# Kernel tuning notes

Hardware: AMD Instinct MI355X
Metric: run time of the kernel (lower is better)

The kernel has to match this reference:

```python
import jax, jax.numpy as jnp
import numpy as np
from jax import lax

T_ITERS = 6
LN_EPS = 1e-5

def layer_norm(x, g, b):
    mu = jnp.mean(x, axis=-1, keepdims=True)
    var = jnp.var(x, axis=-1, keepdims=True)
    return (x - mu) * lax.rsqrt(var + LN_EPS) * g + b

def setup_inputs() -> dict:
    key = jax.random.key(0)
    ks = jax.random.split(key, 12)
    B, C_in, S = 8, 128, 33
    hidden = 2 * C_in          # 256
    dim = 256                  # feat_dim
    N = 64
    w = lambda k, shp, s=0.02: (jax.random.normal(k, shp, jnp.float32) * s)
    return {
        "x": jax.random.normal(ks[0], (B, C_in, S, S, S), jnp.float32),
        "templates_init": jax.random.normal(ks[1], (1, N, dim), jnp.float32),
        "conv_w": w(ks[2], (hidden, C_in, 3, 3, 3)),
        "conv_b": jnp.zeros((hidden,), jnp.float32),
        "Wq": w(ks[3], (dim, dim)),
        "Wk": w(ks[4], (hidden, dim)),
        "Wv": w(ks[5], (hidden, dim)),
        "ln_in_g": jnp.ones((hidden,), jnp.float32), "ln_in_b": jnp.zeros((hidden,), jnp.float32),
        "ln_t_g": jnp.ones((dim,), jnp.float32),    "ln_t_b": jnp.zeros((dim,), jnp.float32),
        "ln_m_g": jnp.ones((dim,), jnp.float32),    "ln_m_b": jnp.zeros((dim,), jnp.float32),
        "W1": w(ks[6], (dim, 2 * dim)), "b1": jnp.zeros((2 * dim,), jnp.float32),
        "W2": w(ks[7], (2 * dim, dim)), "b2": jnp.zeros((dim,), jnp.float32),
    }

def reference(x, templates_init, conv_w, conv_b, Wq, Wk, Wv,
              ln_in_g, ln_in_b, ln_t_g, ln_t_b, ln_m_g, ln_m_b,
              W1, b1, W2, b2):
    # project: Conv3d stride 2, no padding, + ReLU
    h = lax.conv_general_dilated(x, conv_w, window_strides=(2, 2, 2),
                                 padding='VALID',
                                 dimension_numbers=('NCDHW', 'OIDHW', 'NCDHW'))
    h = jax.nn.relu(h + conv_b[None, :, None, None, None])
    B, C, X, Y, Z = h.shape
    dim = templates_init.shape[-1]
    N = templates_init.shape[1]
    scale = dim ** (-0.5)
    tokens = h.reshape(B, C, X * Y * Z).transpose(0, 2, 1)   # (B, L, hidden)
    tokens = layer_norm(tokens, ln_in_g, ln_in_b)
    k = tokens @ Wk                                           # (B, L, dim)
    v = tokens @ Wv                                           # (B, L, dim)
    templates = jnp.broadcast_to(templates_init, (B, N, dim))
    attn = None
    for _ in range(T_ITERS):
        t_prev = templates
        t = layer_norm(templates, ln_t_g, ln_t_b)
        q = (t @ Wq) * scale                                  # (B, N, dim)
        attn_logits = jnp.einsum('bnd,bld->bln', q, k)        # (B, L, N)
        attn = jax.nn.softmax(attn_logits, axis=-1)           # competitive over N
        attn = attn + 1e-8
        attn = attn / jnp.sum(attn, axis=-2, keepdims=True)   # renormalize over L
        templates = t_prev + jnp.einsum('bld,bln->bnd', v, attn)
        m = layer_norm(templates, ln_m_g, ln_m_b)
        templates = templates + (jax.nn.gelu(m @ W1 + b1, approximate=False) @ W2 + b2)
    templates_out = templates.transpose(0, 2, 1)              # (B, dim, N)
    attn_out = attn.transpose(0, 2, 1).reshape(B, N, X, Y, Z)
    return templates_out, attn_out
```

## Files before the change

### kernel.cpp

```cpp
#include <hip/hip_runtime.h>

typedef unsigned short u16;
typedef short s16x8 __attribute__((ext_vector_type(8)));
typedef float f32x4 __attribute__((ext_vector_type(4)));
typedef float f32x4u __attribute__((ext_vector_type(4), aligned(4)));
typedef unsigned short us4 __attribute__((ext_vector_type(4)));

__device__ __forceinline__ float bf2f(u16 v) {
    return __uint_as_float(((unsigned int)v) << 16);
}
__device__ __forceinline__ u16 f2bf(float f) {
    unsigned int u = __float_as_uint(f);
    u = u + 0x7FFFu + ((u >> 16) & 1u);
    return (u16)(u >> 16);
}
__device__ __forceinline__ f32x4 mfma16(s16x8 a, s16x8 b, f32x4 c) {
    return __builtin_amdgcn_mfma_f32_16x16x32_bf16(a, b, c, 0, 0, 0);
}
#define ZERO4 f32x4{0.f, 0.f, 0.f, 0.f}

__global__ void prepack_kernel(const float* __restrict__ conv_w, const float* __restrict__ Wk,
                               const float* __restrict__ Wv, const float* __restrict__ Wq,
                               const float* __restrict__ W1, const float* __restrict__ W2,
                               u16* __restrict__ Bp, u16* __restrict__ WkvP, u16* __restrict__ WqP,
                               u16* __restrict__ W1T, u16* __restrict__ W2T)
{
    int idx = blockIdx.x * 256 + threadIdx.x;
    if (idx < 294912) {
        int n = idx / 1152, g = idx - n * 1152;
        int ic = g / 9, r = g - ic * 9;
        const float* s = conv_w + n * 3456 + ic * 27 + r * 3;
        u16* d = Bp + n * 4608 + g * 4;
        d[0] = f2bf(s[0]); d[1] = f2bf(s[1]); d[2] = f2bf(s[2]); d[3] = 0;
    } else if (idx < 425984) {
        int i = idx - 294912;
        int n = i >> 8, c = i & 255;
        WkvP[i] = f2bf((n < 256) ? Wk[c * 256 + n] : Wv[c * 256 + (n - 256)]);
    } else if (idx < 491520) {
        int i = idx - 425984;
        int n = i >> 8, c = i & 255;
        WqP[i] = f2bf(Wq[c * 256 + n]);
    } else if (idx < 622592) {
        int i = idx - 491520;
        int h = i >> 8, c = i & 255;
        W1T[i] = f2bf(W1[c * 512 + h]);
    } else if (idx < 753664) {
        int i = idx - 622592;
        int dd = i >> 9, h = i & 511;
        W2T[i] = f2bf(W2[h * 256 + dd]);
    }
}

__global__ __launch_bounds__(512, 4) void conv_fused(
    const float* __restrict__ x, const u16* __restrict__ Bp, const float* __restrict__ conv_b,
    const float* __restrict__ ln_g, const float* __restrict__ ln_b, const u16* __restrict__ WkvP,
    u16* __restrict__ kbuf, u16* __restrict__ vT)
{
    __shared__ __align__(16) char smem[38400];
    u16* slab   = (u16*)smem;
    u16* tokbf  = (u16*)smem;
    float* lnred  = (float*)(smem + 33792);
    float* lnstat = (float*)(smem + 37888);

    int blk = blockIdx.x;
    int b = blk >> 6, ox = (blk >> 2) & 15, oyb = blk & 3;
    int tid = threadIdx.x, wid = tid >> 6, lane = tid & 63;
    int quad = lane >> 4, l15 = lane & 15;
    int nbase = wid * 32;

    f32x4 acc[4][2];
    #pragma unroll
    for (int i = 0; i < 4; ++i)
        #pragma unroll
        for (int j = 0; j < 2; ++j) acc[i][j] = ZERO4;

    const u16* bprow0 = Bp + (nbase + l15) * 4608 + quad * 8;
    const u16* bprow1 = bprow0 + 16 * 4608;

    for (int icc = 0; icc < 8; ++icc) {
        __syncthreads();
        {
            f32x4u tv[8];
            int so8[8];
            #pragma unroll
            for (int u = 0; u < 8; ++u) {
                int s = tid + u * 512;
                tv[u] = f32x4u{0.f, 0.f, 0.f, 0.f};
                so8[u] = -1;
                if (s < 3888) {
                    int row = s / 9;
                    int c = s - row * 9;
                    int icl = row / 27;
                    int rr = row - icl * 27;
                    int ixl = rr / 9;
                    int iyl = rr - ixl * 9;
                    const float* xr = x + ((size_t)((b * 128 + icc * 16 + icl) * 33)
                                           + (2 * ox + ixl)) * 1089 + (8 * oyb + iyl) * 33;
                    if (c < 8) tv[u] = *(const f32x4u*)(xr + c * 4);
                    else       tv[u].x = xr[32];
                    so8[u] = row * 36 + c * 4;
                }
            }
            #pragma unroll
            for (int u = 0; u < 8; ++u) {
                if (so8[u] >= 0) {
                    us4 w;
                    w.x = f2bf(tv[u].x); w.y = f2bf(tv[u].y);
                    w.z = f2bf(tv[u].z); w.w = f2bf(tv[u].w);
                    *(us4*)(slab + so8[u]) = w;
                }
            }
        }
        __syncthreads();

        const u16* bk0 = bprow0 + icc * 576;
        const u16* bk1 = bprow1 + icc * 576;
        s16x8 bbA[2], bbB[2];
        bbA[0] = *reinterpret_cast<const s16x8*>(bk0);
// ... 99 lines not shown
    for (int i = 0; i < 4; ++i)
        #pragma unroll
        for (int j = 0; j < 4; ++j) kacc[i][j] = ZERO4;
    int n2 = wid * 64;
    const u16* wp = WkvP + (n2 + l15) * 256 + quad * 8;
    s16x8 wvA[4], wvB[4];
    #pragma unroll
    for (int fn = 0; fn < 4; ++fn) wvA[fn] = *reinterpret_cast<const s16x8*>(wp + fn * 4096);

#define KV_STEP(KK, WREG)                                                           \
    {                                                                               \
        s16x8 a2[4];                                                                \
        _Pragma("unroll")                                                           \
        for (int fm = 0; fm < 4; ++fm)                                              \
            a2[fm] = *reinterpret_cast<const s16x8*>(tokbf + (fm * 16 + l15) * 264  \
                                                     + (KK) * 32 + quad * 8);       \
        _Pragma("unroll")                                                           \
        for (int fn = 0; fn < 4; ++fn)                                              \
            _Pragma("unroll")                                                       \
            for (int fm = 0; fm < 4; ++fm)                                          \
                kacc[fm][fn] = mfma16(a2[fm], (WREG)[fn], kacc[fm][fn]);            \
    }

    #pragma unroll 1
    for (int kc = 0; kc < 8; kc += 2) {
        #pragma unroll
        for (int fn = 0; fn < 4; ++fn)
            wvB[fn] = *reinterpret_cast<const s16x8*>(wp + fn * 4096 + (kc + 1) * 32);
        KV_STEP(kc, wvA)
        if (kc + 2 < 8) {
            #pragma unroll
            for (int fn = 0; fn < 4; ++fn)
                wvA[fn] = *reinterpret_cast<const s16x8*>(wp + fn * 4096 + (kc + 2) * 32);
        }
        KV_STEP(kc + 1, wvB)
    }
#undef KV_STEP

    #pragma unroll
    for (int fm = 0; fm < 4; ++fm)
        #pragma unroll
        for (int r = 0; r < 4; ++r) {
            int l = (ox * 16 + oyb * 4 + fm) * 16 + quad * 4 + r;
            #pragma unroll
            for (int fn = 0; fn < 4; ++fn) {
                int n = n2 + fn * 16 + l15;
                u16 v = f2bf(kacc[fm][fn][r]);
                if (n < 256) kbuf[((b << 12) + l) * 256 + n] = v;
                else         vT[((b * 256 + (n - 256)) << 12) + l] = v;
            }
        }
}

__global__ __launch_bounds__(256) void kQ(
    const float* __restrict__ tinit, float* __restrict__ tpl,
    const float* __restrict__ ln_t_g, const float* __restrict__ ln_t_b,
    const u16* __restrict__ WqP, u16* __restrict__ qbuf)
{
    __shared__ __align__(16) u16 mls[64 * 264];
    __shared__ float pls[64][4][2];
    __shared__ float stat[64][2];
    int b = blockIdx.x, tid = threadIdx.x;
    int m = tid >> 2, part = tid & 3;
    const float* tp = tinit + m * 256 + part * 64;
    float* tg = tpl + (b * 64 + m) * 256 + part * 64;
    float s = 0, q2 = 0;
    for (int i = 0; i < 64; ++i) {
        float v = tp[i];
        tg[i] = v;
        s += v; q2 += v * v;
    }
    pls[m][part][0] = s; pls[m][part][1] = q2;
    __syncthreads();
    if (tid < 64) {
        float ss = 0, qq = 0;
        #pragma unroll
        for (int p = 0; p < 4; ++p) { ss += pls[tid][p][0]; qq += pls[tid][p][1]; }
        float mu = ss * (1.f / 256.f);
        float var = fmaxf(qq * (1.f / 256.f) - mu * mu, 0.f);
        stat[tid][0] = mu; stat[tid][1] = rsqrtf(var + 1e-5f);
    }
    __syncthreads();
    {
        float mu = stat[m][0], rs = stat[m][1];
        for (int i = 0; i < 64; ++i) {
            int d = part * 64 + i;
            mls[m * 264 + d] = f2bf((tp[i] - mu) * rs * ln_t_g[d] + ln_t_b[d]);
        }
    }
    __syncthreads();
    int wid = tid >> 6, lane = tid & 63, quad = lane >> 4, l15 = lane & 15;
    f32x4 qa[4][4];
    #pragma unroll
    for (int i = 0; i < 4; ++i)
        #pragma unroll
        for (int j = 0; j < 4; ++j) qa[i][j] = ZERO4;
    #pragma unroll 1
    for (int kc = 0; kc < 8; ++kc) {
        s16x8 a[4];
        #pragma unroll
        for (int fm = 0; fm < 4; ++fm)
            a[fm] = *reinterpret_cast<const s16x8*>(mls + (fm * 16 + l15) * 264 + kc * 32 + quad * 8);
        #pragma unroll
        for (int fn = 0; fn < 4; ++fn) {
            s16x8 bv = *reinterpret_cast<const s16x8*>(WqP + (wid * 64 + fn * 16 + l15) * 256 + kc * 32 + quad * 8);
            #pragma unroll
            for (int fm = 0; fm < 4; ++fm)
                qa[fm][fn] = mfma16(a[fm], bv, qa[fm][fn]);
        }
    }
    #pragma unroll
    for (int fm = 0; fm < 4; ++fm)
        #pragma unroll
        for (int fn = 0; fn < 4; ++fn)
            #pragma unroll
            for (int r = 0; r < 4; ++r) {
                int mt = fm * 16 + quad * 4 + r;
                int d = wid * 64 + fn * 16 + l15;
                qbuf[(b * 64 + mt) * 256 + d] = f2bf(qa[fm][fn][r] * 0.0625f);
            }
}

__global__ __launch_bounds__(512, 2) void kP(
    const u16* __restrict__ qbuf, const u16* __restrict__ kbuf,
    float* __restrict__ cs_part, u16* __restrict__ attnT)
{
    __shared__ __align__(16) u16 atile[64 * 136];
    __shared__ float colsh[8][64];
    int b = blockIdx.x >> 5, ltg = blockIdx.x & 31;
    int tid = threadIdx.x, wid = tid >> 6, lane = tid & 63;
    int quad = lane >> 4, l15 = lane & 15;
    const u16* qb = qbuf + b * 16384;
    int lrow = ltg * 128 + wid * 16;
    const u16* arow = kbuf + (size_t)((b << 12) + lrow + l15) * 256;
    f32x4 sa[4];
    #pragma unroll
    for (int fn = 0; fn < 4; ++fn) sa[fn] = ZERO4;
    #pragma unroll 1
    for (int kc = 0; kc < 8; ++kc) {
        s16x8 a = *reinterpret_cast<const s16x8*>(arow + kc * 32 + quad * 8);
        #pragma unroll
        for (int fn = 0; fn < 4; ++fn) {
            s16x8 bv = *reinterpret_cast<const s16x8*>(qb + (fn * 16 + l15) * 256 + kc * 32 + quad * 8);
            sa[fn] = mfma16(a, bv, sa[fn]);
        }
    }
    float colp[4] = {0.f, 0.f, 0.f, 0.f};
    #pragma unroll
    for (int r = 0; r < 4; ++r) {
        float mx = fmaxf(fmaxf(sa[0][r], sa[1][r]), fmaxf(sa[2][r], sa[3][r]));
        #pragma unroll
        for (int msk = 1; msk <= 8; msk <<= 1) mx = fmaxf(mx, __shfl_xor(mx, msk, 64));
        float e[4], sum = 0;
        #pragma unroll
        for (int fn = 0; fn < 4; ++fn) { e[fn] = __expf(sa[fn][r] - mx); sum += e[fn]; }
        #pragma unroll
        for (int msk = 1; msk <= 8; msk <<= 1) sum += __shfl_xor(sum, msk, 64);
        float inv = 1.f / sum;
        #pragma unroll
        for (int fn = 0; fn < 4; ++fn) {
            float p = e[fn] * inv + 1e-8f;
            colp[fn] += p;
            atile[(fn * 16 + l15) * 136 + wid * 16 + quad * 4 + r] = f2bf(p);
        }
    }
    #pragma unroll
    for (int fn = 0; fn < 4; ++fn) {
        float c = colp[fn];
        c += __shfl_xor(c, 16, 64);
        c += __shfl_xor(c, 32, 64);
        if (lane < 16) colsh[wid][fn * 16 + lane] = c;
    }
    __syncthreads();
    if (tid < 64) {
        float s = 0;
        #pragma unroll
        for (int w = 0; w < 8; ++w) s += colsh[w][tid];
        cs_part[((b << 5) + ltg) * 64 + tid] = s;
    }
    {
        int n = tid >> 3, lo = (tid & 7) * 16;
        const u16* src = atile + n * 136 + lo;
        u16* dst = attnT + (size_t)((b * 64 + n) << 12) + ltg * 128 + lo;
        *(int4*)(dst)     = *(const int4*)(src);
        *(int4*)(dst + 8) = *(const int4*)(src + 8);
    }
}

__global__ __launch_bounds__(512, 2) void kPV(
    const u16* __restrict__ attnT, const u16* __restrict__ vT, float* __restrict__ delta)
{
    __shared__ float pred[8][64][16];
    int b = blockIdx.x >> 4, dt = blockIdx.x & 15;
    int tid = threadIdx.x, wid = tid >> 6, lane = tid & 63;
    int quad = lane >> 4, l15 = lane & 15;
    const u16* prow = attnT + (size_t)((b * 64 + l15) << 12) + wid * 512 + quad * 8;
    const u16* vrow = vT + (size_t)((b * 256 + dt * 16 + l15) << 12) + wid * 512 + quad * 8;
    f32x4 acc[4];
    #pragma unroll
    for (int i = 0; i < 4; ++i) acc[i] = ZERO4;
    #pragma unroll 1
    for (int kc = 0; kc < 16; ++kc) {
        s16x8 bv = *reinterpret_cast<const s16x8*>(vrow + kc * 32);
        #pragma unroll
        for (int fm = 0; fm < 4; ++fm) {
            s16x8 a = *reinterpret_cast<const s16x8*>(prow + (fm << 16) + kc * 32);
            acc[fm] = mfma16(a, bv, acc[fm]);
        }
    }
    #pragma unroll
    for (int fm = 0; fm < 4; ++fm)
        #pragma unroll
        for (int r = 0; r < 4; ++r)
            pred[wid][fm * 16 + quad * 4 + r][l15] = acc[fm][r];
    __syncthreads();
    for (int i = tid; i < 1024; i += 512) {
        int n = i >> 4, d = i & 15;
        float s = 0;
        #pragma unroll
        for (int w = 0; w < 8; ++w) s += pred[w][n][d];
        delta[(size_t)(b * 64 + n) * 256 + dt * 16 + d] = s;
    }
}

__global__ __launch_bounds__(256) void kT(
    float* __restrict__ tpl, const float* __restrict__ delta, const float* __restrict__ cs_part,
    float* __restrict__ colsum,
    const float* __restrict__ ln_m_g, const float* __restrict__ ln_m_b,
    const u16* __restrict__ W1T, const float* __restrict__ b1,
    const u16* __restrict__ W2T, const float* __restrict__ b2,
    const float* __restrict__ ln_t_g, const float* __restrict__ ln_t_b,
    const u16* __restrict__ WqP, u16* __restrict__ qbuf,
    int last, float* __restrict__ out0)
{
    __shared__ __align__(16) u16 mls[16 * 264];
    __shared__ __align__(16) u16 hid[16 * 520];
    __shared__ float pls[16][16][2];
    __shared__ float stat[16][2];
    __shared__ float lnr2[4][16][2];
    __shared__ float csh[16];
    int b = blockIdx.x >> 2, mg = blockIdx.x & 3;
    int m0 = mg * 16;
    int tid = threadIdx.x, wid = tid >> 6, lane = tid & 63;
    int quad = lane >> 4, l15 = lane & 15;
    if (tid < 16) {
        float s = 0;
        #pragma unroll
        for (int g = 0; g < 32; ++g) s += cs_part[((b << 5) + g) * 64 + m0 + tid];
        csh[tid] = 1.f / s;
        if (last) colsum[b * 64 + m0 + tid] = s;
    }
    __syncthreads();
    {
        int ml = tid >> 4, part = tid & 15;
        float cinv = csh[ml];
        float* tg = tpl + (b * 64 + m0 + ml) * 256 + part * 16;
        const float* dg = delta + (b * 64 + m0 + ml) * 256 + part * 16;
        float vbuf[16];
        float s = 0, q2 = 0;
        #pragma unroll
        for (int i = 0; i < 16; ++i) {
            float v = tg[i] + dg[i] * cinv;
            vbuf[i] = v; s += v; q2 += v * v;
        }
        pls[ml][part][0] = s; pls[ml][part][1] = q2;
        __syncthreads();
        if (tid < 16) {
            float ss = 0, qq = 0;
            #pragma unroll
            for (int p = 0; p < 16; ++p) { ss += pls[tid][p][0]; qq += pls[tid][p][1]; }
            float mu = ss * (1.f / 256.f);
            float var = fmaxf(qq * (1.f / 256.f) - mu * mu, 0.f);
            stat[tid][0] = mu; stat[tid][1] = rsqrtf(var + 1e-5f);
        }
        __syncthreads();
        float mu = stat[ml][0], rs = stat[ml][1];
        #pragma unroll
        for (int i = 0; i < 16; ++i) {
            int d = part * 16 + i;
            tg[i] = vbuf[i];
            mls[ml * 264 + d] = f2bf((vbuf[i] - mu) * rs * ln_m_g[d] + ln_m_b[d]);
        }
    }
    __syncthreads();
    {
        f32x4 ha[8];
        #pragma unroll
        for (int j = 0; j < 8; ++j) ha[j] = ZERO4;
        #pragma unroll 1
        for (int kc = 0; kc < 8; ++kc) {
            s16x8 a = *reinterpret_cast<const s16x8*>(mls + l15 * 264 + kc * 32 + quad * 8);
            #pragma unroll
            for (int fn = 0; fn < 8; ++fn) {
                s16x8 bv = *reinterpret_cast<const s16x8*>(W1T + (wid * 128 + fn * 16 + l15) * 256 + kc * 32 + quad * 8);
                ha[fn] = mfma16(a, bv, ha[fn]);
            }
        }
        #pragma unroll
        for (int fn = 0; fn < 8; ++fn) {
            int nh = wid * 128 + fn * 16 + l15;
            float bb = b1[nh];
            #pragma unroll
            for (int r = 0; r < 4; ++r) {
                float v = ha[fn][r] + bb;
                v = 0.5f * v * (1.f + erff(v * 0.70710678118654752f));
                hid[(quad * 4 + r) * 520 + nh] = f2bf(v);
            }
        }
    }
    __syncthreads();
    {
        f32x4 oa[4];
        #pragma unroll
        for (int j = 0; j < 4; ++j) oa[j] = ZERO4;
        #pragma unroll 1
        for (int kc = 0; kc < 16; ++kc) {
            s16x8 a = *reinterpret_cast<const s16x8*>(hid + l15 * 520 + kc * 32 + quad * 8);
            #pragma unroll
            for (int fn = 0; fn < 4; ++fn) {
                s16x8 bv = *reinterpret_cast<const s16x8*>(W2T + (wid * 64 + fn * 16 + l15) * 512 + kc * 32 + quad * 8);
                oa[fn] = mfma16(a, bv, oa[fn]);
            }
        }
        #pragma unroll
        for (int fn = 0; fn < 4; ++fn) {
            int d = wid * 64 + fn * 16 + l15;
            float bb = b2[d];
            #pragma unroll
            for (int r = 0; r < 4; ++r) {
                int mm = quad * 4 + r;
                oa[fn][r] += bb + tpl[(b * 64 + m0 + mm) * 256 + d];
            }
        }
        #pragma unroll
        for (int r = 0; r < 4; ++r) {
            float s = oa[0][r] + oa[1][r] + oa[2][r] + oa[3][r];
            float q2 = oa[0][r] * oa[0][r] + oa[1][r] * oa[1][r]
                     + oa[2][r] * oa[2][r] + oa[3][r] * oa[3][r];
            #pragma unroll
            for (int msk = 1; msk <= 8; msk <<= 1) {
                s  += __shfl_xor(s, msk, 64);
                q2 += __shfl_xor(q2, msk, 64);
            }
            if (l15 == 0) {
                lnr2[wid][quad * 4 + r][0] = s;
                lnr2[wid][quad * 4 + r][1] = q2;
            }
        }
        __syncthreads();
        if (tid < 16) {
            float ss = 0, qq = 0;
            #pragma unroll
            for (int w = 0; w < 4; ++w) { ss += lnr2[w][tid][0]; qq += lnr2[w][tid][1]; }
            float mu = ss * (1.f / 256.f);
            float var = fmaxf(qq * (1.f / 256.f) - mu * mu, 0.f);
            stat[tid][0] = mu; stat[tid][1] = rsqrtf(var + 1e-5f);
        }
        __syncthreads();
        #pragma unroll
        for (int fn = 0; fn < 4; ++fn) {
            int d = wid * 64 + fn * 16 + l15;
            float gg = last ? 0.f : ln_t_g[d];
            float bt = last ? 0.f : ln_t_b[d];
            #pragma unroll
            for (int r = 0; r < 4; ++r) {
                int mm = quad * 4 + r;
                float v = oa[fn][r];
                tpl[(b * 64 + m0 + mm) * 256 + d] = v;
                if (last) {
                    out0[(b * 256 + d) * 64 + m0 + mm] = v;
                } else {
                    mls[mm * 264 + d] = f2bf((v - stat[mm][0]) * stat[mm][1] * gg + bt);
                }
            }
        }
    }
    if (!last) {
        __syncthreads();
        f32x4 qa[4];
        #pragma unroll
        for (int j = 0; j < 4; ++j) qa[j] = ZERO4;
        #pragma unroll 1
        for (int kc = 0; kc < 8; ++kc) {
            s16x8 a = *reinterpret_cast<const s16x8*>(mls + l15 * 264 + kc * 32 + quad * 8);
            #pragma unroll
            for (int fn = 0; fn < 4; ++fn) {
                s16x8 bv = *reinterpret_cast<const s16x8*>(WqP + (wid * 64 + fn * 16 + l15) * 256 + kc * 32 + quad * 8);
                qa[fn] = mfma16(a, bv, qa[fn]);
            }
        }
        #pragma unroll
        for (int fn = 0; fn < 4; ++fn)
            #pragma unroll
            for (int r = 0; r < 4; ++r) {
                int mt = m0 + quad * 4 + r;
                int d = wid * 64 + fn * 16 + l15;
                qbuf[(b * 64 + mt) * 256 + d] = f2bf(qa[fn][r] * 0.0625f);
            }
    }
}

__global__ void kE(const u16* __restrict__ attnT, const float* __restrict__ colsum,
                   float* __restrict__ out1)
{
    int idx = blockIdx.x * 256 + threadIdx.x;
    int e = idx * 4;
    int b = e >> 18, n = (e >> 12) & 63;
    float ci = 1.f / colsum[b * 64 + n];
    const u16* s = attnT + e;
    f32x4 o;
    o.x = bf2f(s[0]) * ci; o.y = bf2f(s[1]) * ci;
    o.z = bf2f(s[2]) * ci; o.w = bf2f(s[3]) * ci;
    *(f32x4*)(out1 + e) = o;
}

extern "C" void kernel_launch(void* const* d_in, const int* in_sizes, int n_in,
                              void* d_out, int out_size, void* d_ws, size_t ws_size,
                              hipStream_t stream)
{
    const float* x       = (const float*)d_in[0];
    const float* tinit   = (const float*)d_in[1];
    const float* conv_w  = (const float*)d_in[2];
    const float* conv_b  = (const float*)d_in[3];
    const float* Wq      = (const float*)d_in[4];
    const float* Wk      = (const float*)d_in[5];
    const float* Wv      = (const float*)d_in[6];
    const float* ln_in_g = (const float*)d_in[7];
    const float* ln_in_b = (const float*)d_in[8];
    const float* ln_t_g  = (const float*)d_in[9];
    const float* ln_t_b  = (const float*)d_in[10];
    const float* ln_m_g  = (const float*)d_in[11];
    const float* ln_m_b  = (const float*)d_in[12];
    const float* W1      = (const float*)d_in[13];
    const float* b1      = (const float*)d_in[14];
    const float* W2      = (const float*)d_in[15];
    const float* b2      = (const float*)d_in[16];

    char* ws = (char*)d_ws;
    u16* Bp       = (u16*)(ws + 0);
    u16* WkvP     = (u16*)(ws + 2359296);
    u16* WqP      = (u16*)(ws + 2621440);
    u16* W1T      = (u16*)(ws + 2752512);
    u16* W2T      = (u16*)(ws + 3014656);
    u16* kbuf     = (u16*)(ws + 3276800);
    u16* vT       = (u16*)(ws + 20054016);
    u16* qbuf     = (u16*)(ws + 36831232);
    u16* attnT    = (u16*)(ws + 37093376);
    float* colsum = (float*)(ws + 41287680);
    float* tpl    = (float*)(ws + 41289728);
    float* delta  = (float*)(ws + 41814016);
    float* cs_part= (float*)(ws + 42338304);

    float* out0 = (float*)d_out;
    float* out1 = out0 + 131072;

    prepack_kernel<<<2944, 256, 0, stream>>>(conv_w, Wk, Wv, Wq, W1, W2, Bp, WkvP, WqP, W1T, W2T);
    conv_fused<<<512, 512, 0, stream>>>(x, Bp, conv_b, ln_in_g, ln_in_b, WkvP, kbuf, vT);
    kQ<<<8, 256, 0, stream>>>(tinit, tpl, ln_t_g, ln_t_b, WqP, qbuf);
    for (int it = 0; it < 6; ++it) {
        int last = (it == 5) ? 1 : 0;
        kP<<<256, 512, 0, stream>>>(qbuf, kbuf, cs_part, attnT);
        kPV<<<128, 512, 0, stream>>>(attnT, vT, delta);
        kT<<<32, 256, 0, stream>>>(tpl, delta, cs_part, colsum, ln_m_g, ln_m_b, W1T, b1, W2T, b2,
                                   ln_t_g, ln_t_b, WqP, qbuf, last, out0);
    }
    kE<<<2048, 256, 0, stream>>>(attnT, colsum, out1);
}
```

Measured before the change: 820.7 us.

## Fuse iteration kernels into one persistent kernel with grid-wide barriers

Replaces the per-iteration kQ/kP/kPV/kT launches and the final kE with a single persistent kernel of 256 blocks that moves between phases using a hand-rolled atomic grid barrier. The PV product and the template MLP appear to be merged into the 32-block phase, so the delta buffer is dropped. The goal is to remove about 20 kernel launches and their gaps from a small, latency-bound loop. The barrier depends on all 256 blocks being co-resident (launch bounds of 512 threads with 2 blocks per CU), and phases that use only 8 or 32 blocks leave most of the grid idle while it spins.

```diff
diff --git a/kernel.cpp b/kernel.cpp
--- a/kernel.cpp
+++ b/kernel.cpp
@@ -18,6 +18,27 @@
     return __builtin_amdgcn_mfma_f32_16x16x32_bf16(a, b, c, 0, 0, 0);
 }
 #define ZERO4 f32x4{0.f, 0.f, 0.f, 0.f}
+
+__device__ __align__(128) unsigned g_cnt;
+__device__ __align__(128) unsigned g_gen;
+
+__device__ __forceinline__ void gbar(int nblk) {
+    __syncthreads();
+    if (threadIdx.x == 0) {
+        __threadfence();
+        unsigned g = __hip_atomic_load(&g_gen, __ATOMIC_RELAXED, __HIP_MEMORY_SCOPE_AGENT);
+        unsigned a = __hip_atomic_fetch_add(&g_cnt, 1u, __ATOMIC_ACQ_REL, __HIP_MEMORY_SCOPE_AGENT);
+        if (a == (unsigned)(nblk - 1)) {
+            __hip_atomic_store(&g_cnt, 0u, __ATOMIC_RELAXED, __HIP_MEMORY_SCOPE_AGENT);
+            __hip_atomic_store(&g_gen, g + 1u, __ATOMIC_RELEASE, __HIP_MEMORY_SCOPE_AGENT);
+        } else {
+            while (__hip_atomic_load(&g_gen, __ATOMIC_ACQUIRE, __HIP_MEMORY_SCOPE_AGENT) == g)
+                __builtin_amdgcn_s_sleep(2);
+        }
+        __threadfence();
+    }
+    __syncthreads();
+}
 
 __global__ void prepack_kernel(const float* __restrict__ conv_w, const float* __restrict__ Wk,
                                const float* __restrict__ Wv, const float* __restrict__ Wq,
@@ -269,366 +290,351 @@
         }
 }
 
-__global__ __launch_bounds__(256) void kQ(
+__global__ __launch_bounds__(512, 2) void fused_iter(
     const float* __restrict__ tinit, float* __restrict__ tpl,
     const float* __restrict__ ln_t_g, const float* __restrict__ ln_t_b,
-    const u16* __restrict__ WqP, u16* __restrict__ qbuf)
+    const float* __restrict__ ln_m_g, const float* __restrict__ ln_m_b,
+    const u16* __restrict__ WqP, const u16* __restrict__ W1T, const float* __restrict__ b1,
+    const u16* __restrict__ W2T, const float* __restrict__ b2,
+    const u16* __restrict__ kbuf, const u16* __restrict__ vT,
+    u16* __restrict__ qbuf, u16* __restrict__ attnT,
+    float* __restrict__ cs_part, float* __restrict__ colsum,
+    float* __restrict__ out0, float* __restrict__ out1)
 {
-    __shared__ __align__(16) u16 mls[64 * 264];
-    __shared__ float pls[64][4][2];
-    __shared__ float stat[64][2];
-    int b = blockIdx.x, tid = threadIdx.x;
-    int m = tid >> 2, part = tid & 3;
-    const float* tp = tinit + m * 256 + part * 64;
-    float* tg = tpl + (b * 64 + m) * 256 + part * 64;
-    float s = 0, q2 = 0;
-    for (int i = 0; i < 64; ++i) {
-        float v = tp[i];
-        tg[i] = v;
-        s += v; q2 += v * v;
-    }
-    pls[m][part][0] = s; pls[m][part][1] = q2;
-    __syncthreads();
-    if (tid < 64) {
-        float ss = 0, qq = 0;
-        #pragma unroll
-        for (int p = 0; p < 4; ++p) { ss += pls[tid][p][0]; qq += pls[tid][p][1]; }
-        float mu = ss * (1.f / 256.f);
-        float var = fmaxf(qq * (1.f / 256.f) - mu * mu, 0.f);
-        stat[tid][0] = mu; stat[tid][1] = rsqrtf(var + 1e-5f);
-    }
-    __syncthreads();
-    {
-        float mu = stat[m][0], rs = stat[m][1];
-        for (int i = 0; i < 64; ++i) {
-            int d = part * 64 + i;
-            mls[m * 264 + d] = f2bf((tp[i] - mu) * rs * ln_t_g[d] + ln_t_b[d]);
-        }
-    }
-    __syncthreads();
-    int wid = tid >> 6, lane = tid & 63, quad = lane >> 4, l15 = lane & 15;
-    f32x4 qa[4][4];
-    #pragma unroll
-    for (int i = 0; i < 4; ++i)
-        #pragma unroll
-        for (int j = 0; j < 4; ++j) qa[i][j] = ZERO4;
-    #pragma unroll 1
-    for (int kc = 0; kc < 8; ++kc) {
-        s16x8 a[4];
-        #pragma unroll
-        for (int fm = 0; fm < 4; ++fm)
-            a[fm] = *reinterpret_cast<const s16x8*>(mls + (fm * 16 + l15) * 264 + kc * 32 + quad * 8);
-        #pragma unroll
-        for (int fn = 0; fn < 4; ++fn) {
-            s16x8 bv = *reinterpret_cast<const s16x8*>(WqP + (wid * 64 + fn * 16 + l15) * 256 + kc * 32 + quad * 8);
-            #pragma unroll
-            for (int fm = 0; fm < 4; ++fm)
-                qa[fm][fn] = mfma16(a[fm], bv, qa[fm][fn]);
-        }
-    }
-    #pragma unroll
-    for (int fm = 0; fm < 4; ++fm)
-        #pragma unroll
-        for (int fn = 0; fn < 4; ++fn)
-            #pragma unroll
-            for (int r = 0; r < 4; ++r) {
-                int mt = fm * 16 + quad * 4 + r;
-                int d = wid * 64 + fn * 16 + l15;
-                qbuf[(b * 64 + mt) * 256 + d] = f2bf(qa[fm][fn][r] * 0.0625f);
-            }
-}
-
-__global__ __launch_bounds__(512, 2) void kP(
-    const u16* __restrict__ qbuf, const u16* __restrict__ kbuf,
-    float* __restrict__ cs_part, u16* __restrict__ attnT)
-{
-    __shared__ __align__(16) u16 atile[64 * 136];
-    __shared__ float colsh[8][64];
-    int b = blockIdx.x >> 5, ltg = blockIdx.x & 31;
-    int tid = threadIdx.x, wid = tid >> 6, lane = tid & 63;
+    __shared__ __align__(16) char smem[46848];
+    const int nblk = gridDim.x;
+    int blk = blockIdx.x, tid = threadIdx.x;
+    int wid = tid >> 6, lane = tid & 63;
     int quad = lane >> 4, l15 = lane & 15;
-    const u16* qb = qbuf + b * 16384;
-    int lrow = ltg * 128 + wid * 16;
-    const u16* arow = kbuf + (size_t)((b << 12) + lrow + l15) * 256;
-    f32x4 sa[4];
-    #pragma unroll
-    for (int fn = 0; fn < 4; ++fn) sa[fn] = ZERO4;
-    #pragma unroll 1
-    for (int kc = 0; kc < 8; ++kc) {
-        s16x8 a = *reinterpret_cast<const s16x8*>(arow + kc * 32 + quad * 8);
-        #pragma unroll
-        for (int fn = 0; fn < 4; ++fn) {
-            s16x8 bv = *reinterpret_cast<const s16x8*>(qb + (fn * 16 + l15) * 256 + kc * 32 + quad * 8);
-            sa[fn] = mfma16(a, bv, sa[fn]);
-        }
-    }
-    float colp[4] = {0.f, 0.f, 0.f, 0.f};
-    #pragma unroll
-    for (int r = 0; r < 4; ++r) {
-        float mx = fmaxf(fmaxf(sa[0][r], sa[1][r]), fmaxf(sa[2][r], sa[3][r]));
-        #pragma unroll
-        for (int msk = 1; msk <= 8; msk <<= 1) mx = fmaxf(mx, __shfl_xor(mx, msk, 64));
-        float e[4], sum = 0;
-        #pragma unroll
-        for (int fn = 0; fn < 4; ++fn) { e[fn] = __expf(sa[fn][r] - mx); sum += e[fn]; }
-        #pragma unroll
-        for (int msk = 1; msk <= 8; msk <<= 1) sum += __shfl_xor(sum, msk, 64);
-        float inv = 1.f / sum;
-        #pragma unroll
-        for (int fn = 0; fn < 4; ++fn) {
-            float p = e[fn] * inv + 1e-8f;
-            colp[fn] += p;
-            atile[(fn * 16 + l15) * 136 + wid * 16 + quad * 4 + r] = f2bf(p);
-        }
-    }
-    #pragma unroll
-    for (int fn = 0; fn < 4; ++fn) {
-        float c = colp[fn];
-        c += __shfl_xor(c, 16, 64);
-        c += __shfl_xor(c, 32, 64);
-        if (lane < 16) colsh[wid][fn * 16 + lane] = c;
-    }
-    __syncthreads();
-    if (tid < 64) {
-        float s = 0;
-        #pragma unroll
-        for (int w = 0; w < 8; ++w) s += colsh[w][tid];
-        cs_part[((b << 5) + ltg) * 64 + tid] = s;
-    }
-    {
-        int n = tid >> 3, lo = (tid & 7) * 16;
-        const u16* src = atile + n * 136 + lo;
-        u16* dst = attnT + (size_t)((b * 64 + n) << 12) + ltg * 128 + lo;
-        *(int4*)(dst)     = *(const int4*)(src);
-        *(int4*)(dst + 8) = *(const int4*)(src + 8);
-    }
-}
-
-__global__ __launch_bounds__(512, 2) void kPV(
-    const u16* __restrict__ attnT, const u16* __restrict__ vT, float* __restrict__ delta)
-{
-    __shared__ float pred[8][64][16];
-    int b = blockIdx.x >> 4, dt = blockIdx.x & 15;
-    int tid = threadIdx.x, wid = tid >> 6, lane = tid & 63;
-    int quad = lane >> 4, l15 = lane & 15;
-    const u16* prow = attnT + (size_t)((b * 64 + l15) << 12) + wid * 512 + quad * 8;
-    const u16* vrow = vT + (size_t)((b * 256 + dt * 16 + l15) << 12) + wid * 512 + quad * 8;
-    f32x4 acc[4];
-    #pragma unroll
-    for (int i = 0; i < 4; ++i) acc[i] = ZERO4;
-    #pragma unroll 1
-    for (int kc = 0; kc < 16; ++kc) {
-        s16x8 bv = *reinterpret_cast<const s16x8*>(vrow + kc * 32);
-        #pragma unroll
-        for (int fm = 0; fm < 4; ++fm) {
-            s16x8 a = *reinterpret_cast<const s16x8*>(prow + (fm << 16) + kc * 32);
-            acc[fm] = mfma16(a, bv, acc[fm]);
-        }
-    }
-    #pragma unroll
-    for (int fm = 0; fm < 4; ++fm)
-        #pragma unroll
-        for (int r = 0; r < 4; ++r)
-            pred[wid][fm * 16 + quad * 4 + r][l15] = acc[fm][r];
-    __syncthreads();
-    for (int i = tid; i < 1024; i += 512) {
-        int n = i >> 4, d = i & 15;
-        float s = 0;
-        #pragma unroll
-        for (int w = 0; w < 8; ++w) s += pred[w][n][d];
-        delta[(size_t)(b * 64 + n) * 256 + dt * 16 + d] = s;
-    }
-}
-
-__global__ __launch_bounds__(256) void kT(
-    float* __restrict__ tpl, const float* __restrict__ delta, const float* __restrict__ cs_part,
-    float* __restrict__ colsum,
-    const float* __restrict__ ln_m_g, const float* __restrict__ ln_m_b,
-    const u16* __restrict__ W1T, const float* __restrict__ b1,
-    const u16* __restrict__ W2T, const float* __restrict__ b2,
-    const float* __restrict__ ln_t_g, const float* __restrict__ ln_t_b,
-    const u16* __restrict__ WqP, u16* __restrict__ qbuf,
-    int last, float* __restrict__ out0)
-{
-    __shared__ __align__(16) u16 mls[16 * 264];
-    __shared__ __align__(16) u16 hid[16 * 520];
-    __shared__ float pls[16][16][2];
-    __shared__ float stat[16][2];
-    __shared__ float lnr2[4][16][2];
-    __shared__ float csh[16];
-    int b = blockIdx.x >> 2, mg = blockIdx.x & 3;
-    int m0 = mg * 16;
-    int tid = threadIdx.x, wid = tid >> 6, lane = tid & 63;
-    int quad = lane >> 4, l15 = lane & 15;
-    if (tid < 16) {
-        float s = 0;
-        #pragma unroll
-        for (int g = 0; g < 32; ++g) s += cs_part[((b << 5) + g) * 64 + m0 + tid];
-        csh[tid] = 1.f / s;
-        if (last) colsum[b * 64 + m0 + tid] = s;
-    }
-    __syncthreads();
-    {
-        int ml = tid >> 4, part = tid & 15;
-        float cinv = csh[ml];
-        float* tg = tpl + (b * 64 + m0 + ml) * 256 + part * 16;
-        const float* dg = delta + (b * 64 + m0 + ml) * 256 + part * 16;
-        float vbuf[16];
+
+    if (blk < 8) {
+        u16* mlsQ = (u16*)smem;
+        float* plsQ = (float*)(smem + 33792);
+        float* statQ = (float*)(smem + 37888);
+        int b = blk;
+        int m = tid >> 3, part = tid & 7;
+        const float* tp = tinit + m * 256 + part * 32;
+        float* tg = tpl + (b * 64 + m) * 256 + part * 32;
         float s = 0, q2 = 0;
         #pragma unroll
-        for (int i = 0; i < 16; ++i) {
-            float v = tg[i] + dg[i] * cinv;
-            vbuf[i] = v; s += v; q2 += v * v;
-        }
-        pls[ml][part][0] = s; pls[ml][part][1] = q2;
+        for (int i = 0; i < 32; ++i) {
+            float v = tp[i];
+            tg[i] = v;
+            s += v; q2 += v * v;
+        }
+        plsQ[(m * 8 + part) * 2 + 0] = s; plsQ[(m * 8 + part) * 2 + 1] = q2;
         __syncthreads();
-        if (tid < 16) {
+        if (tid < 64) {
             float ss = 0, qq = 0;
             #pragma unroll
-            for (int p = 0; p < 16; ++p) { ss += pls[tid][p][0]; qq += pls[tid][p][1]; }
+            for (int p = 0; p < 8; ++p) { ss += plsQ[(tid * 8 + p) * 2]; qq += plsQ[(tid * 8 + p) * 2 + 1]; }
             float mu = ss * (1.f / 256.f);
             float var = fmaxf(qq * (1.f / 256.f) - mu * mu, 0.f);
-            stat[tid][0] = mu; stat[tid][1] = rsqrtf(var + 1e-5f);
+            statQ[tid * 2] = mu; statQ[tid * 2 + 1] = rsqrtf(var + 1e-5f);
         }
         __syncthreads();
-        float mu = stat[ml][0], rs = stat[ml][1];
-        #pragma unroll
-        for (int i = 0; i < 16; ++i) {
-            int d = part * 16 + i;
-            tg[i] = vbuf[i];
-            mls[ml * 264 + d] = f2bf((vbuf[i] - mu) * rs * ln_m_g[d] + ln_m_b[d]);
-        }
-    }
-    __syncthreads();
-    {
-        f32x4 ha[8];
-        #pragma unroll
-        for (int j = 0; j < 8; ++j) ha[j] = ZERO4;
+        {
+            float mu = statQ[m * 2], rs = statQ[m * 2 + 1];
+            #pragma unroll
+            for (int i = 0; i < 32; ++i) {
+                int d = part * 32 + i;
+                mlsQ[m * 264 + d] = f2bf((tp[i] - mu) * rs * ln_t_g[d] + ln_t_b[d]);
+            }
+        }
+        __syncthreads();
+        f32x4 qa[4][2];
+        #pragma unroll
+        for (int i = 0; i < 4; ++i)
+            #pragma unroll
+            for (int j = 0; j < 2; ++j) qa[i][j] = ZERO4;
         #pragma unroll 1
         for (int kc = 0; kc < 8; ++kc) {
-            s16x8 a = *reinterpret_cast<const s16x8*>(mls + l15 * 264 + kc * 32 + quad * 8);
-            #pragma unroll
-            for (int fn = 0; fn < 8; ++fn) {
-                s16x8 bv = *reinterpret_cast<const s16x8*>(W1T + (wid * 128 + fn * 16 + l15) * 256 + kc * 32 + quad * 8);
-                ha[fn] = mfma16(a, bv, ha[fn]);
-            }
-        }
-        #pragma unroll
-        for (int fn = 0; fn < 8; ++fn) {
-            int nh = wid * 128 + fn * 16 + l15;
-            float bb = b1[nh];
+            s16x8 a[4];
+            #pragma unroll
+            for (int fm = 0; fm < 4; ++fm)
+                a[fm] = *reinterpret_cast<const s16x8*>(mlsQ + (fm * 16 + l15) * 264 + kc * 32 + quad * 8);
+            #pragma unroll
+            for (int fn = 0; fn < 2; ++fn) {
+                s16x8 bv = *reinterpret_cast<const s16x8*>(WqP + (wid * 32 + fn * 16 + l15) * 256 + kc * 32 + quad * 8);
+                #pragma unroll
+                for (int fm = 0; fm < 4; ++fm)
+                    qa[fm][fn] = mfma16(a[fm], bv, qa[fm][fn]);
+            }
+        }
+        #pragma unroll
+        for (int fm = 0; fm < 4; ++fm)
+            #pragma unroll
+            for (int fn = 0; fn < 2; ++fn)
+                #pragma unroll
+                for (int r = 0; r < 4; ++r) {
+                    int mt = fm * 16 + quad * 4 + r;
+                    int d = wid * 32 + fn * 16 + l15;
+                    qbuf[(b * 64 + mt) * 256 + d] = f2bf(qa[fm][fn][r] * 0.0625f);
+                }
+    }
+    gbar(nblk);
+
+    for (int it = 0; it < 6; ++it) {
+        int last = (it == 5) ? 1 : 0;
+        {
+            u16* atile = (u16*)smem;
+            float* colsh = (float*)(smem + 17408);
+            int b = blk >> 5, ltg = blk & 31;
+            const u16* qb = qbuf + b * 16384;
+            int lrow = ltg * 128 + wid * 16;
+            const u16* arow = kbuf + (size_t)((b << 12) + lrow + l15) * 256;
+            f32x4 sa[4];
+            #pragma unroll
+            for (int fn = 0; fn < 4; ++fn) sa[fn] = ZERO4;
+            #pragma unroll 1
+            for (int kc = 0; kc < 8; ++kc) {
+                s16x8 a = *reinterpret_cast<const s16x8*>(arow + kc * 32 + quad * 8);
+                #pragma unroll
+                for (int fn = 0; fn < 4; ++fn) {
+                    s16x8 bv = *reinterpret_cast<const s16x8*>(qb + (fn * 16 + l15) * 256 + kc * 32 + quad * 8);
+                    sa[fn] = mfma16(a, bv, sa[fn]);
+                }
+            }
+            float colp[4] = {0.f, 0.f, 0.f, 0.f};
             #pragma unroll
             for (int r = 0; r < 4; ++r) {
-                float v = ha[fn][r] + bb;
-                v = 0.5f * v * (1.f + erff(v * 0.70710678118654752f));
-                hid[(quad * 4 + r) * 520 + nh] = f2bf(v);
-            }
-        }
-    }
-    __syncthreads();
+                float mx = fmaxf(fmaxf(sa[0][r], sa[1][r]), fmaxf(sa[2][r], sa[3][r]));
+                #pragma unroll
+                for (int msk = 1; msk <= 8; msk <<= 1) mx = fmaxf(mx, __shfl_xor(mx, msk, 64));
+                float e[4], sum = 0;
+                #pragma unroll
+                for (int fn = 0; fn < 4; ++fn) { e[fn] = __expf(sa[fn][r] - mx); sum += e[fn]; }
+                #pragma unroll
+                for (int msk = 1; msk <= 8; msk <<= 1) sum += __shfl_xor(sum, msk, 64);
+                float inv = 1.f / sum;
+                #pragma unroll
+                for (int fn = 0; fn < 4; ++fn) {
+                    float p = e[fn] * inv + 1e-8f;
+                    colp[fn] += p;
+                    atile[(fn * 16 + l15) * 136 + wid * 16 + quad * 4 + r] = f2bf(p);
+                }
+            }
+            #pragma unroll
+            for (int fn = 0; fn < 4; ++fn) {
+                float c = colp[fn];
+                c += __shfl_xor(c, 16, 64);
+                c += __shfl_xor(c, 32, 64);
+                if (lane < 16) colsh[wid * 64 + fn * 16 + lane] = c;
+            }
+            __syncthreads();
+            if (tid < 64) {
+                float s = 0;
+                #pragma unroll
+                for (int w = 0; w < 8; ++w) s += colsh[w * 64 + tid];
+                cs_part[((b << 5) + ltg) * 64 + tid] = s;
+            }
+            {
+                int n = tid >> 3, lo = (tid & 7) * 16;
+                const u16* src = atile + n * 136 + lo;
+                u16* dst = attnT + (size_t)((b * 64 + n) << 12) + ltg * 128 + lo;
+                *(int4*)(dst)     = *(const int4*)(src);
+                *(int4*)(dst + 8) = *(const int4*)(src + 8);
+            }
+        }
+        gbar(nblk);
+
+        if (blk < 32) {
+            float* dsh  = (float*)smem;
+            u16* mls    = (u16*)(smem + 16384);
+            u16* hid    = (u16*)(smem + 24832);
+            float* pls  = (float*)(smem + 41472);
+            float* stat = (float*)(smem + 45568);
+            float* lnr2 = (float*)(smem + 45696);
+            float* cshT = (float*)(smem + 46720);
+            int b = blk >> 2, mg = blk & 3, m0 = mg * 16;
+            if (tid < 16) {
+                float s = 0;
+                #pragma unroll
+                for (int g = 0; g < 32; ++g) s += cs_part[((b << 5) + g) * 64 + m0 + tid];
+                cshT[tid] = 1.f / s;
+                if (last) colsum[b * 64 + m0 + tid] = s;
+            }
+            {
+                const u16* prow = attnT + ((size_t)(b * 64 + m0 + l15) << 12) + quad * 8;
+                const u16* vrow = vT + ((size_t)(b * 256 + wid * 32 + l15) << 12) + quad * 8;
+                f32x4 pacc[2];
+                pacc[0] = ZERO4; pacc[1] = ZERO4;
+                #pragma unroll 2
+                for (int kc = 0; kc < 128; ++kc) {
+                    s16x8 a  = *reinterpret_cast<const s16x8*>(prow + kc * 32);
+                    s16x8 b0 = *reinterpret_cast<const s16x8*>(vrow + kc * 32);
+                    s16x8 b1 = *reinterpret_cast<const s16x8*>(vrow + (16 << 12) + kc * 32);
+                    pacc[0] = mfma16(a, b0, pacc[0]);
+                    pacc[1] = mfma16(a, b1, pacc[1]);
+                }
+                #pragma unroll
+                for (int fn = 0; fn < 2; ++fn)
+                    #pragma unroll
+                    for (int r = 0; r < 4; ++r)
+                        dsh[(quad * 4 + r) * 256 + wid * 32 + fn * 16 + l15] = pacc[fn][r];
+            }
+            __syncthreads();
+            {
+                int ml = tid >> 5, part = tid & 31;
+                float cinv = cshT[ml];
+                float* tg = tpl + (b * 64 + m0 + ml) * 256 + part * 8;
+                float vbuf[8];
+                float s = 0, q2 = 0;
+                #pragma unroll
+                for (int i = 0; i < 8; ++i) {
+                    float v = tg[i] + dsh[ml * 256 + part * 8 + i] * cinv;
+                    vbuf[i] = v; s += v; q2 += v * v;
+                }
+                pls[(ml * 32 + part) * 2 + 0] = s; pls[(ml * 32 + part) * 2 + 1] = q2;
+                __syncthreads();
+                if (tid < 16) {
+                    float ss = 0, qq = 0;
+                    #pragma unroll
+                    for (int p = 0; p < 32; ++p) { ss += pls[(tid * 32 + p) * 2]; qq += pls[(tid * 32 + p) * 2 + 1]; }
+                    float mu = ss * (1.f / 256.f);
+                    float var = fmaxf(qq * (1.f / 256.f) - mu * mu, 0.f);
+                    stat[tid * 2] = mu; stat[tid * 2 + 1] = rsqrtf(var + 1e-5f);
+                }
+                __syncthreads();
+                float mu = stat[ml * 2], rs = stat[ml * 2 + 1];
+                #pragma unroll
+                for (int i = 0; i < 8; ++i) {
+                    int d = part * 8 + i;
+                    tg[i] = vbuf[i];
+                    mls[ml * 264 + d] = f2bf((vbuf[i] - mu) * rs * ln_m_g[d] + ln_m_b[d]);
+                }
+            }
+            __syncthreads();
+            {
+                f32x4 ha[4];
+                #pragma unroll
+                for (int j = 0; j < 4; ++j) ha[j] = ZERO4;
+                #pragma unroll 1
+                for (int kc = 0; kc < 8; ++kc) {
+                    s16x8 a = *reinterpret_cast<const s16x8*>(mls + l15 * 264 + kc * 32 + quad * 8);
+                    #pragma unroll
+                    for (int fn = 0; fn < 4; ++fn) {
+                        s16x8 bv = *reinterpret_cast<const s16x8*>(W1T + (wid * 64 + fn * 16 + l15) * 256 + kc * 32 + quad * 8);
+                        ha[fn] = mfma16(a, bv, ha[fn]);
+                    }
+                }
+                #pragma unroll
+                for (int fn = 0; fn < 4; ++fn) {
+                    int nh = wid * 64 + fn * 16 + l15;
+                    float bb = b1[nh];
+                    #pragma unroll
+                    for (int r = 0; r < 4; ++r) {
+                        float v = ha[fn][r] + bb;
+                        v = 0.5f * v * (1.f + erff(v * 0.70710678118654752f));
+                        hid[(quad * 4 + r) * 520 + nh] = f2bf(v);
+                    }
+                }
+            }
+            __syncthreads();
+            {
+                f32x4 oa[2];
+                oa[0] = ZERO4; oa[1] = ZERO4;
+                #pragma unroll 1
+                for (int kc = 0; kc < 16; ++kc) {
+                    s16x8 a = *reinterpret_cast<const s16x8*>(hid + l15 * 520 + kc * 32 + quad * 8);
+                    #pragma unroll
+                    for (int fn = 0; fn < 2; ++fn) {
+                        s16x8 bv = *reinterpret_cast<const s16x8*>(W2T + (wid * 32 + fn * 16 + l15) * 512 + kc * 32 + quad * 8);
+                        oa[fn] = mfma16(a, bv, oa[fn]);
+                    }
+                }
+                #pragma unroll
+                for (int fn = 0; fn < 2; ++fn) {
+                    int d = wid * 32 + fn * 16 + l15;
+                    float bb = b2[d];
+                    #pragma unroll
+                    for (int r = 0; r < 4; ++r) {
+                        int mm = quad * 4 + r;
+                        oa[fn][r] += bb + tpl[(b * 64 + m0 + mm) * 256 + d];
+                    }
+                }
+                #pragma unroll
+                for (int r = 0; r < 4; ++r) {
+                    float s = oa[0][r] + oa[1][r];
+                    float q2 = oa[0][r] * oa[0][r] + oa[1][r] * oa[1][r];
+                    #pragma unroll
+                    for (int msk = 1; msk <= 8; msk <<= 1) {
+                        s  += __shfl_xor(s, msk, 64);
+                        q2 += __shfl_xor(q2, msk, 64);
+                    }
+                    if (l15 == 0) {
+                        lnr2[(wid * 16 + quad * 4 + r) * 2 + 0] = s;
+                        lnr2[(wid * 16 + quad * 4 + r) * 2 + 1] = q2;
+                    }
+                }
+                __syncthreads();
+                if (tid < 16) {
+                    float ss = 0, qq = 0;
+                    #pragma unroll
+                    for (int w = 0; w < 8; ++w) { ss += lnr2[(w * 16 + tid) * 2]; qq += lnr2[(w * 16 + tid) * 2 + 1]; }
+                    float mu = ss * (1.f / 256.f);
+                    float var = fmaxf(qq * (1.f / 256.f) - mu * mu, 0.f);
+                    stat[tid * 2] = mu; stat[tid * 2 + 1] = rsqrtf(var + 1e-5f);
+                }
+                __syncthreads();
+                #pragma unroll
+                for (int fn = 0; fn < 2; ++fn) {
+                    int d = wid * 32 + fn * 16 + l15;
+                    float gg = last ? 0.f : ln_t_g[d];
+                    float bt = last ? 0.f : ln_t_b[d];
+                    #pragma unroll
+                    for (int r = 0; r < 4; ++r) {
+                        int mm = quad * 4 + r;
+                        float v = oa[fn][r];
+                        tpl[(b * 64 + m0 + mm) * 256 + d] = v;
+                        if (last) {
+                            out0[(b * 256 + d) * 64 + m0 + mm] = v;
+                        } else {
+                            mls[mm * 264 + d] = f2bf((v - stat[mm * 2]) * stat[mm * 2 + 1] * gg + bt);
+                        }
+                    }
+                }
+            }
+            if (!last) {
+                __syncthreads();
+                f32x4 qa[2];
+                qa[0] = ZERO4; qa[1] = ZERO4;
+                #pragma unroll 1
+                for (int kc = 0; kc < 8; ++kc) {
+                    s16x8 a = *reinterpret_cast<const s16x8*>(mls + l15 * 264 + kc * 32 + quad * 8);
+                    #pragma unroll
+                    for (int fn = 0; fn < 2; ++fn) {
+                        s16x8 bv = *reinterpret_cast<const s16x8*>(WqP + (wid * 32 + fn * 16 + l15) * 256 + kc * 32 + quad * 8);
+                        qa[fn] = mfma16(a, bv, qa[fn]);
+                    }
+                }
+                #pragma unroll
+                for (int fn = 0; fn < 2; ++fn)
+                    #pragma unroll
+                    for (int r = 0; r < 4; ++r) {
+                        int mt = m0 + quad * 4 + r;
+                        int d = wid * 32 + fn * 16 + l15;
+                        qbuf[(b * 64 + mt) * 256 + d] = f2bf(qa[fn][r] * 0.0625f);
+                    }
+            }
+        }
+        gbar(nblk);
+    }
+
     {
-        f32x4 oa[4];
-        #pragma unroll
-        for (int j = 0; j < 4; ++j) oa[j] = ZERO4;
-        #pragma unroll 1
-        for (int kc = 0; kc < 16; ++kc) {
-            s16x8 a = *reinterpret_cast<const s16x8*>(hid + l15 * 520 + kc * 32 + quad * 8);
-            #pragma unroll
-            for (int fn = 0; fn < 4; ++fn) {
-                s16x8 bv = *reinterpret_cast<const s16x8*>(W2T + (wid * 64 + fn * 16 + l15) * 512 + kc * 32 + quad * 8);
-                oa[fn] = mfma16(a, bv, oa[fn]);
-            }
-        }
-        #pragma unroll
-        for (int fn = 0; fn < 4; ++fn) {
-            int d = wid * 64 + fn * 16 + l15;
-            float bb = b2[d];
-            #pragma unroll
-            for (int r = 0; r < 4; ++r) {
-                int mm = quad * 4 + r;
-                oa[fn][r] += bb + tpl[(b * 64 + m0 + mm) * 256 + d];
-            }
-        }
-        #pragma unroll
-        for (int r = 0; r < 4; ++r) {
-            float s = oa[0][r] + oa[1][r] + oa[2][r] + oa[3][r];
-            float q2 = oa[0][r] * oa[0][r] + oa[1][r] * oa[1][r]
-                     + oa[2][r] * oa[2][r] + oa[3][r] * oa[3][r];
-            #pragma unroll
-            for (int msk = 1; msk <= 8; msk <<= 1) {
-                s  += __shfl_xor(s, msk, 64);
-                q2 += __shfl_xor(q2, msk, 64);
-            }
-            if (l15 == 0) {
-                lnr2[wid][quad * 4 + r][0] = s;
-                lnr2[wid][quad * 4 + r][1] = q2;
-            }
-        }
-        __syncthreads();
-        if (tid < 16) {
-            float ss = 0, qq = 0;
-            #pragma unroll
-            for (int w = 0; w < 4; ++w) { ss += lnr2[w][tid][0]; qq += lnr2[w][tid][1]; }
-            float mu = ss * (1.f / 256.f);
-            float var = fmaxf(qq * (1.f / 256.f) - mu * mu, 0.f);
-            stat[tid][0] = mu; stat[tid][1] = rsqrtf(var + 1e-5f);
-        }
-        __syncthreads();
-        #pragma unroll
-        for (int fn = 0; fn < 4; ++fn) {
-            int d = wid * 64 + fn * 16 + l15;
-            float gg = last ? 0.f : ln_t_g[d];
-            float bt = last ? 0.f : ln_t_b[d];
-            #pragma unroll
-            for (int r = 0; r < 4; ++r) {
-                int mm = quad * 4 + r;
-                float v = oa[fn][r];
-                tpl[(b * 64 + m0 + mm) * 256 + d] = v;
-                if (last) {
-                    out0[(b * 256 + d) * 64 + m0 + mm] = v;
-                } else {
-                    mls[mm * 264 + d] = f2bf((v - stat[mm][0]) * stat[mm][1] * gg + bt);
-                }
-            }
-        }
-    }
-    if (!last) {
-        __syncthreads();
-        f32x4 qa[4];
-        #pragma unroll
-        for (int j = 0; j < 4; ++j) qa[j] = ZERO4;
-        #pragma unroll 1
-        for (int kc = 0; kc < 8; ++kc) {
-            s16x8 a = *reinterpret_cast<const s16x8*>(mls + l15 * 264 + kc * 32 + quad * 8);
-            #pragma unroll
-            for (int fn = 0; fn < 4; ++fn) {
-                s16x8 bv = *reinterpret_cast<const s16x8*>(WqP + (wid * 64 + fn * 16 + l15) * 256 + kc * 32 + quad * 8);
-                qa[fn] = mfma16(a, bv, qa[fn]);
-            }
-        }
-        #pragma unroll
-        for (int fn = 0; fn < 4; ++fn)
-            #pragma unroll
-            for (int r = 0; r < 4; ++r) {
-                int mt = m0 + quad * 4 + r;
-                int d = wid * 64 + fn * 16 + l15;
-                qbuf[(b * 64 + mt) * 256 + d] = f2bf(qa[fn][r] * 0.0625f);
-            }
-    }
-}
-
-__global__ void kE(const u16* __restrict__ attnT, const float* __restrict__ colsum,
-                   float* __restrict__ out1)
-{
-    int idx = blockIdx.x * 256 + threadIdx.x;
-    int e = idx * 4;
-    int b = e >> 18, n = (e >> 12) & 63;
-    float ci = 1.f / colsum[b * 64 + n];
-    const u16* s = attnT + e;
-    f32x4 o;
-    o.x = bf2f(s[0]) * ci; o.y = bf2f(s[1]) * ci;
-    o.z = bf2f(s[2]) * ci; o.w = bf2f(s[3]) * ci;
-    *(f32x4*)(out1 + e) = o;
+        #pragma unroll
+        for (int j = 0; j < 4; ++j) {
+            int idx = blk * 512 + tid + j * 131072;
+            int e = idx * 4;
+            int b = e >> 18, n = (e >> 12) & 63;
+            float ci = 1.f / colsum[b * 64 + n];
+            const u16* s = attnT + e;
+            f32x4 o;
+            o.x = bf2f(s[0]) * ci; o.y = bf2f(s[1]) * ci;
+            o.z = bf2f(s[2]) * ci; o.w = bf2f(s[3]) * ci;
+            *(f32x4*)(out1 + e) = o;
+        }
+    }
 }
 
 extern "C" void kernel_launch(void* const* d_in, const int* in_sizes, int n_in,
@@ -665,21 +671,14 @@
     u16* attnT    = (u16*)(ws + 37093376);
     float* colsum = (float*)(ws + 41287680);
     float* tpl    = (float*)(ws + 41289728);
-    float* delta  = (float*)(ws + 41814016);
-    float* cs_part= (float*)(ws + 42338304);
+    float* cs_part= (float*)(ws + 41814016);
 
     float* out0 = (float*)d_out;
     float* out1 = out0 + 131072;
 
     prepack_kernel<<<2944, 256, 0, stream>>>(conv_w, Wk, Wv, Wq, W1, W2, Bp, WkvP, WqP, W1T, W2T);
     conv_fused<<<512, 512, 0, stream>>>(x, Bp, conv_b, ln_in_g, ln_in_b, WkvP, kbuf, vT);
-    kQ<<<8, 256, 0, stream>>>(tinit, tpl, ln_t_g, ln_t_b, WqP, qbuf);
-    for (int it = 0; it < 6; ++it) {
-        int last = (it == 5) ? 1 : 0;
-        kP<<<256, 512, 0, stream>>>(qbuf, kbuf, cs_part, attnT);
-        kPV<<<128, 512, 0, stream>>>(attnT, vT, delta);
-        kT<<<32, 256, 0, stream>>>(tpl, delta, cs_part, colsum, ln_m_g, ln_m_b, W1T, b1, W2T, b2,
-                                   ln_t_g, ln_t_b, WqP, qbuf, last, out0);
-    }
-    kE<<<2048, 256, 0, stream>>>(attnT, colsum, out1);
-}
+    fused_iter<<<256, 512, 0, stream>>>(tinit, tpl, ln_t_g, ln_t_b, ln_m_g, ln_m_b,
+                                        WqP, W1T, b1, W2T, b2, kbuf, vT,
+                                        qbuf, attnT, cs_part, colsum, out0, out1);
+}
```

Measured after the change: 2.841 ms. 3.46x slower.

## Interleave batch index across blocks for XCD locality and prefetch PV operands

Applied to the files above, without the earlier changes.

Remaps blockIdx in the conv, kP, kPV, kT and kE kernels so that the batch index is the fastest-varying component (blk & 7). On MI355X, blocks are dispatched round-robin across 8 XCDs, so each batch's data should stay in one XCD's L2. kPV also gets a double-buffered register prefetch of the attention and V fragments, and kP's k-loop is unrolled by 2, both to hide global load latency. The risk is higher register pressure in kPV.

```diff
diff --git a/kernel.cpp b/kernel.cpp
--- a/kernel.cpp
+++ b/kernel.cpp
@@ -63,7 +63,7 @@
     float* lnstat = (float*)(smem + 37888);
 
     int blk = blockIdx.x;
-    int b = blk >> 6, ox = (blk >> 2) & 15, oyb = blk & 3;
+    int b = blk & 7, ox = (blk >> 5) & 15, oyb = (blk >> 3) & 3;
     int tid = threadIdx.x, wid = tid >> 6, lane = tid & 63;
     int quad = lane >> 4, l15 = lane & 15;
     int nbase = wid * 32;
@@ -344,7 +344,7 @@
 {
     __shared__ __align__(16) u16 atile[64 * 136];
     __shared__ float colsh[8][64];
-    int b = blockIdx.x >> 5, ltg = blockIdx.x & 31;
+    int b = blockIdx.x & 7, ltg = blockIdx.x >> 3;
     int tid = threadIdx.x, wid = tid >> 6, lane = tid & 63;
     int quad = lane >> 4, l15 = lane & 15;
     const u16* qb = qbuf + b * 16384;
@@ -353,7 +353,7 @@
     f32x4 sa[4];
     #pragma unroll
     for (int fn = 0; fn < 4; ++fn) sa[fn] = ZERO4;
-    #pragma unroll 1
+    #pragma unroll 2
     for (int kc = 0; kc < 8; ++kc) {
         s16x8 a = *reinterpret_cast<const s16x8*>(arow + kc * 32 + quad * 8);
         #pragma unroll
@@ -408,7 +408,7 @@
     const u16* __restrict__ attnT, const u16* __restrict__ vT, float* __restrict__ delta)
 {
     __shared__ float pred[8][64][16];
-    int b = blockIdx.x >> 4, dt = blockIdx.x & 15;
+    int b = blockIdx.x & 7, dt = blockIdx.x >> 3;
     int tid = threadIdx.x, wid = tid >> 6, lane = tid & 63;
     int quad = lane >> 4, l15 = lane & 15;
     const u16* prow = attnT + (size_t)((b * 64 + l15) << 12) + wid * 512 + quad * 8;
@@ -416,14 +416,26 @@
     f32x4 acc[4];
     #pragma unroll
     for (int i = 0; i < 4; ++i) acc[i] = ZERO4;
+    s16x8 aA[4], bA, aB[4], bB;
+    bA = *reinterpret_cast<const s16x8*>(vrow);
+    #pragma unroll
+    for (int fm = 0; fm < 4; ++fm) aA[fm] = *reinterpret_cast<const s16x8*>(prow + (fm << 16));
     #pragma unroll 1
-    for (int kc = 0; kc < 16; ++kc) {
-        s16x8 bv = *reinterpret_cast<const s16x8*>(vrow + kc * 32);
-        #pragma unroll
-        for (int fm = 0; fm < 4; ++fm) {
-            s16x8 a = *reinterpret_cast<const s16x8*>(prow + (fm << 16) + kc * 32);
-            acc[fm] = mfma16(a, bv, acc[fm]);
-        }
+    for (int kc = 0; kc < 16; kc += 2) {
+        bB = *reinterpret_cast<const s16x8*>(vrow + (kc + 1) * 32);
+        #pragma unroll
+        for (int fm = 0; fm < 4; ++fm)
+            aB[fm] = *reinterpret_cast<const s16x8*>(prow + (fm << 16) + (kc + 1) * 32);
+        #pragma unroll
+        for (int fm = 0; fm < 4; ++fm) acc[fm] = mfma16(aA[fm], bA, acc[fm]);
+        if (kc + 2 < 16) {
+            bA = *reinterpret_cast<const s16x8*>(vrow + (kc + 2) * 32);
+            #pragma unroll
+            for (int fm = 0; fm < 4; ++fm)
+                aA[fm] = *reinterpret_cast<const s16x8*>(prow + (fm << 16) + (kc + 2) * 32);
+        }
+        #pragma unroll
+        for (int fm = 0; fm < 4; ++fm) acc[fm] = mfma16(aB[fm], bB, acc[fm]);
     }
     #pragma unroll
     for (int fm = 0; fm < 4; ++fm)
@@ -456,7 +468,7 @@
     __shared__ float stat[16][2];
     __shared__ float lnr2[4][16][2];
     __shared__ float csh[16];
-    int b = blockIdx.x >> 2, mg = blockIdx.x & 3;
+    int b = blockIdx.x & 7, mg = blockIdx.x >> 3;
     int m0 = mg * 16;
     int tid = threadIdx.x, wid = tid >> 6, lane = tid & 63;
     int quad = lane >> 4, l15 = lane & 15;
@@ -620,9 +632,10 @@
 __global__ void kE(const u16* __restrict__ attnT, const float* __restrict__ colsum,
                    float* __restrict__ out1)
 {
-    int idx = blockIdx.x * 256 + threadIdx.x;
-    int e = idx * 4;
-    int b = e >> 18, n = (e >> 12) & 63;
+    int blk = blockIdx.x;
+    int b = blk & 7, r8 = blk >> 3;
+    int e = (b << 18) + (r8 << 10) + threadIdx.x * 4;
+    int n = (e >> 12) & 63;
     float ci = 1.f / colsum[b * 64 + n];
     const u16* s = attnT + e;
     f32x4 o;
```

After: 806.3 us. No clear change (-1.8%).
